# Performance work log

Hardware: AMD Instinct MI355X
Metric: run time of the kernel (lower is better)

## Reference

```python
import jax, jax.numpy as jnp
import numpy as np


def setup_inputs() -> dict:
    key = jax.random.key(0)
    kq, kk, kv = jax.random.split(key, 3)
    shape = (4, 16, 2048, 128)  # [B, H, S, D]
    return {
        "query": jax.random.normal(kq, shape, dtype=jnp.float32),
        "key": jax.random.normal(kk, shape, dtype=jnp.float32),
        "value": jax.random.normal(kv, shape, dtype=jnp.float32),
    }


def reference(query, key, value):
    # NOTE: the original torch code computes math.sqrt(d) but immediately
    # overwrites it with d itself, so the scale is 1/D (not 1/sqrt(D)).
    d = query.shape[-1]
    score = jnp.einsum("bhqd,bhkd->bhqk", query, key) / d  # [B,H,S,S]
    attn = jax.nn.softmax(score, axis=-1)
    return jnp.einsum("bhqk,bhkd->bhqd", attn, value)
```

## Files before the change

### kernel.cpp

```cpp
#include <hip/hip_runtime.h>
#include <stdint.h>

typedef __bf16 bf16x8 __attribute__((ext_vector_type(8)));
typedef __bf16 bf16x2 __attribute__((ext_vector_type(2)));
typedef float  f32x4  __attribute__((ext_vector_type(4)));

#define DEVI __device__ __forceinline__

constexpr int Bc = 4, Hc = 16, Ss = 2048, Dd = 128;
constexpr int BH = Bc * Hc;
constexpr int BM = 128;
constexpr int BN = 32;
constexpr int NTIL = Ss / BN;
constexpr int LDP = 40;
constexpr float SCALE = 1.0f / 128.0f;

constexpr int TILE_B = BN * Dd * 2;
constexpr int SK_OFF = 0;
constexpr int SV_OFF = 2 * TILE_B;
constexpr int SP_OFF = 4 * TILE_B;
constexpr int LDS_BYTES = SP_OFF + BM * LDP * 2;
static_assert(LDS_BYTES <= 54000, "need 3 blocks/CU");

DEVI unsigned short f2bf_bits(float x) {
  unsigned u = __builtin_bit_cast(unsigned, x);
  u += 0x7fffu + ((u >> 16) & 1u);
  return (unsigned short)(u >> 16);
}
DEVI __bf16 f2bf(float x) {
  unsigned short b = f2bf_bits(x);
  return __builtin_bit_cast(__bf16, b);
}

DEVI void gload_lds16(const void* g, void* l) {
  __builtin_amdgcn_global_load_lds(
      (const __attribute__((address_space(1))) unsigned*)(uintptr_t)g,
      (__attribute__((address_space(3))) unsigned*)(unsigned)(uintptr_t)l,
      16, 0, 0);
}

__global__ void k_conv_bf16(const float* __restrict__ in, __bf16* __restrict__ out,
                            int n4) {
  int i = blockIdx.x * blockDim.x + threadIdx.x;
  const int stride = gridDim.x * blockDim.x;
  for (; i < n4; i += stride) {
    float4 v = ((const float4*)in)[i];
    ushort4 o;
    o.x = f2bf_bits(v.x); o.y = f2bf_bits(v.y);
    o.z = f2bf_bits(v.z); o.w = f2bf_bits(v.w);
    ((ushort4*)out)[i] = o;
  }
}

__global__ void k_vtrans(const float* __restrict__ v, __bf16* __restrict__ vt) {
  constexpr int LDT = 130;
  __shared__ __bf16 tile[64 * LDT];
  const int bh = blockIdx.y;
  const int s0 = blockIdx.x * 64;
  const int u = threadIdx.x;
  const float4* src = (const float4*)(v + ((size_t)bh * Ss + s0) * Dd);
  #pragma unroll
  for (int i = 0; i < 8; i++) {
    int f = i * 256 + u;
    int row = f >> 5;
    int c4 = (f & 31) << 2;
    float4 x = src[f];
    tile[row * LDT + c4 + 0] = f2bf(x.x);
    tile[row * LDT + c4 + 1] = f2bf(x.y);
    tile[row * LDT + c4 + 2] = f2bf(x.z);
    tile[row * LDT + c4 + 3] = f2bf(x.w);
  }
  __syncthreads();
  const int c = u & 7;
  const int dl = u >> 3;
  #pragma unroll
  for (int it = 0; it < 4; it++) {
    const int d = it * 32 + dl;
    bf16x8 o;
    #pragma unroll
    for (int e = 0; e < 8; e++) o[e] = tile[(c * 8 + e) * LDT + d];
    *(bf16x8*)(vt + ((size_t)bh * Dd + d) * Ss + s0 + c * 8) = o;
  }
}

__launch_bounds__(256, 3)
__global__ void k_flash(const float* __restrict__ Q, const __bf16* __restrict__ Kb,
                        const __bf16* __restrict__ Vt, float* __restrict__ O) {
  __shared__ __align__(16) char lds[LDS_BYTES];
  unsigned short* sP = (unsigned short*)(lds + SP_OFF);

  const int tid = threadIdx.x;
  const int w = tid >> 6;
  const int lane = tid & 63;
  const int quad = lane >> 4;
  const int l16 = lane & 15;

  const int bx = blockIdx.x;
  const int bh = bx & (BH - 1);
  const int q0 = (bx >> 6) * BM;

  bf16x8 qa[2][4];
  {
    const float* qb = Q + ((size_t)bh * Ss + q0 + w * 32) * Dd;
    #pragma unroll
    for (int mt = 0; mt < 2; mt++)
      #pragma unroll
      for (int kk = 0; kk < 4; kk++) {
        const float* p = qb + (mt * 16 + l16) * Dd + kk * 32 + quad * 8;
        float4 a = ((const float4*)p)[0];
        float4 b = ((const float4*)p)[1];
        bf16x8 f;
        f[0] = f2bf(a.x * SCALE); f[1] = f2bf(a.y * SCALE);
        f[2] = f2bf(a.z * SCALE); f[3] = f2bf(a.w * SCALE);
        f[4] = f2bf(b.x * SCALE); f[5] = f2bf(b.y * SCALE);
        f[6] = f2bf(b.z * SCALE); f[7] = f2bf(b.w * SCALE);
        qa[mt][kk] = f;
      }
  }

  f32x4 acc[2][8];
  #pragma unroll
  for (int mt = 0; mt < 2; mt++)
    #pragma unroll
    for (int dt = 0; dt < 8; dt++)
      acc[mt][dt] = (f32x4){0.f, 0.f, 0.f, 0.f};

  float lacc[2] = {0.f, 0.f};

  const __bf16* kbh = Kb + (size_t)bh * Ss * Dd;
  const __bf16* vbh = Vt + (size_t)bh * Ss * Dd;

  const char* gp[4];
  unsigned lo[4];
  int ginc;
  if (w < 2) {
    #pragma unroll
    for (int i = 0; i < 4; i++) {
      const int fk = w * 4 + i, kk = fk >> 1, nt = fk & 1;
      gp[i] = (const char*)(kbh + (size_t)(nt * 16 + l16) * Dd + kk * 32 + quad * 8);
      lo[i] = (unsigned)(SK_OFF + fk * 1024 + lane * 16);
    }
    ginc = BN * Dd * 2;
  } else {
    #pragma unroll
    for (int i = 0; i < 4; i++) {
      const int dt = (w - 2) * 4 + i;
      gp[i] = (const char*)(vbh + (size_t)(dt * 16 + l16) * Ss + quad * 8);
      lo[i] = (unsigned)(SV_OFF + dt * 1024 + lane * 16);
    }
    ginc = BN * 2;
  }

  #pragma unroll
  for (int i = 0; i < 4; i++) gload_lds16(gp[i], lds + lo[i]);
  #pragma unroll
  for (int i = 0; i < 4; i++) gp[i] += ginc;
  __syncthreads();

  unsigned cur = 0;
  for (int t = 0; t < NTIL; t++) {
    if (t < NTIL - 1) {
      const unsigned nb = (cur ^ 1u) * (unsigned)TILE_B;
      #pragma unroll
      for (int i = 0; i < 4; i++) gload_lds16(gp[i], lds + lo[i] + nb);
      #pragma unroll
      for (int i = 0; i < 4; i++) gp[i] += ginc;
    }
    const char* bK = lds + SK_OFF + cur * TILE_B;
    const char* bV = lds + SV_OFF + cur * TILE_B;

    f32x4 sc[2][2];
    #pragma unroll
    for (int mt = 0; mt < 2; mt++)
      #pragma unroll
      for (int nt = 0; nt < 2; nt++)
        sc[mt][nt] = (f32x4){0.f, 0.f, 0.f, 0.f};
    __builtin_amdgcn_s_setprio(1);
    #pragma unroll
    for (int kk = 0; kk < 4; kk++)
      #pragma unroll
      for (int nt = 0; nt < 2; nt++) {
        bf16x8 bk = *(const bf16x8*)(bK + (kk * 2 + nt) * 1024 + lane * 16);
        sc[0][nt] = __builtin_amdgcn_mfma_f32_16x16x32_bf16(bk, qa[0][kk], sc[0][nt], 0, 0, 0);
        sc[1][nt] = __builtin_amdgcn_mfma_f32_16x16x32_bf16(bk, qa[1][kk], sc[1][nt], 0, 0, 0);
      }
    __builtin_amdgcn_s_setprio(0);

    #pragma unroll
    for (int mt = 0; mt < 2; mt++)
      #pragma unroll
      for (int nt = 0; nt < 2; nt++) {
        float p0 = __expf(sc[mt][nt][0]);
        float p1 = __expf(sc[mt][nt][1]);
        float p2 = __expf(sc[mt][nt][2]);
        float p3 = __expf(sc[mt][nt][3]);
        lacc[mt] += (p0 + p1) + (p2 + p3);
        bf16x2 ba, bb;
        ba[0] = (__bf16)p0; ba[1] = (__bf16)p1;
        bb[0] = (__bf16)p2; bb[1] = (__bf16)p3;
        uint2 pw;
        pw.x = __builtin_bit_cast(unsigned, ba);
        pw.y = __builtin_bit_cast(unsigned, bb);
        *(uint2*)(sP + (w * 32 + mt * 16 + l16) * LDP + nt * 16 + quad * 4) = pw;
      }

    bf16x8 pa[2];
    #pragma unroll
    for (int mt = 0; mt < 2; mt++)
      pa[mt] = *(const bf16x8*)((const char*)sP +
               (size_t)((w * 32 + mt * 16 + l16) * LDP + quad * 8) * 2);
    __builtin_amdgcn_s_setprio(1);
    #pragma unroll
    for (int dt = 0; dt < 8; dt++) {
      bf16x8 bv = *(const bf16x8*)(bV + dt * 1024 + lane * 16);
      acc[0][dt] = __builtin_amdgcn_mfma_f32_16x16x32_bf16(pa[0], bv, acc[0][dt], 0, 0, 0);
      acc[1][dt] = __builtin_amdgcn_mfma_f32_16x16x32_bf16(pa[1], bv, acc[1][dt], 0, 0, 0);
    }
    __builtin_amdgcn_s_setprio(0);

    __syncthreads();
    cur ^= 1u;
  }

  float inv_l[2][4];
  #pragma unroll
  for (int mt = 0; mt < 2; mt++) {
    float l = lacc[mt];
    l += __shfl_xor(l, 16);
    l += __shfl_xor(l, 32);
    #pragma unroll
    for (int r = 0; r < 4; r++) {
      float lr = __shfl(l, (lane & 48) | (quad * 4 + r));
      inv_l[mt][r] = 1.0f / lr;
    }
  }

  float* ob = O + ((size_t)bh * Ss + q0 + w * 32) * Dd;
  #pragma unroll
  for (int mt = 0; mt < 2; mt++)
    #pragma unroll
    for (int r = 0; r < 4; r++) {
      const float inv = inv_l[mt][r];
      const int row = mt * 16 + quad * 4 + r;
      #pragma unroll
      for (int dt = 0; dt < 8; dt++)
        ob[row * Dd + dt * 16 + l16] = acc[mt][dt][r] * inv;
    }
}

extern "C" void kernel_launch(void* const* d_in, const int* in_sizes, int n_in,
                              void* d_out, int out_size, void* d_ws, size_t ws_size,
                              hipStream_t stream) {
  const float* Q = (const float*)d_in[0];
  const float* K = (const float*)d_in[1];
  const float* V = (const float*)d_in[2];
  float* O = (float*)d_out;
  const size_t elems = (size_t)BH * Ss * Dd;
  __bf16* Kb = (__bf16*)d_ws;
  __bf16* Vt = Kb + elems;

  k_conv_bf16<<<4096, 256, 0, stream>>>(K, Kb, (int)(elems / 4));
  k_vtrans<<<dim3(Ss / 64, BH), 256, 0, stream>>>(V, Vt);
  k_flash<<<dim3((Ss / BM) * BH), 256, 0, stream>>>(Q, Kb, Vt, O);
}
```

Measured before the change: 363.2 us.

## Fuse prep kernels, swizzle P tile, use exp2 and target four blocks per CU

```diff
diff --git a/kernel.cpp b/kernel.cpp
--- a/kernel.cpp
+++ b/kernel.cpp
@@ -12,15 +12,14 @@
 constexpr int BM = 128;
 constexpr int BN = 32;
 constexpr int NTIL = Ss / BN;
-constexpr int LDP = 40;
-constexpr float SCALE = 1.0f / 128.0f;
+constexpr float SCALE = 1.44269504088896340736f / 128.0f;
 
 constexpr int TILE_B = BN * Dd * 2;
 constexpr int SK_OFF = 0;
 constexpr int SV_OFF = 2 * TILE_B;
 constexpr int SP_OFF = 4 * TILE_B;
-constexpr int LDS_BYTES = SP_OFF + BM * LDP * 2;
-static_assert(LDS_BYTES <= 54000, "need 3 blocks/CU");
+constexpr int LDS_BYTES = SP_OFF + BM * BN * 2;
+static_assert(LDS_BYTES <= 40960, "need 4 blocks/CU (160 KiB / 4)");
 
 DEVI unsigned short f2bf_bits(float x) {
   unsigned u = __builtin_bit_cast(unsigned, x);
@@ -31,6 +30,8 @@
   unsigned short b = f2bf_bits(x);
   return __builtin_bit_cast(__bf16, b);
 }
+
+DEVI float exp2_hw(float x) { return __builtin_amdgcn_exp2f(x); }
 
 DEVI void gload_lds16(const void* g, void* l) {
   __builtin_amdgcn_global_load_lds(
@@ -39,25 +40,28 @@
       16, 0, 0);
 }
 
-__global__ void k_conv_bf16(const float* __restrict__ in, __bf16* __restrict__ out,
-                            int n4) {
-  int i = blockIdx.x * blockDim.x + threadIdx.x;
-  const int stride = gridDim.x * blockDim.x;
-  for (; i < n4; i += stride) {
-    float4 v = ((const float4*)in)[i];
-    ushort4 o;
-    o.x = f2bf_bits(v.x); o.y = f2bf_bits(v.y);
-    o.z = f2bf_bits(v.z); o.w = f2bf_bits(v.w);
-    ((ushort4*)out)[i] = o;
-  }
-}
-
-__global__ void k_vtrans(const float* __restrict__ v, __bf16* __restrict__ vt) {
+__global__ void k_prep(const float* __restrict__ kin, __bf16* __restrict__ kout,
+                       const float* __restrict__ v, __bf16* __restrict__ vt) {
   constexpr int LDT = 130;
   __shared__ __bf16 tile[64 * LDT];
-  const int bh = blockIdx.y;
-  const int s0 = blockIdx.x * 64;
+  const int bx = blockIdx.x;
   const int u = threadIdx.x;
+  if (bx >= 2048) {
+    constexpr int N4 = (BH * Ss * Dd) / 4;
+    int i = (bx - 2048) * 256 + u;
+    const int stride = 2048 * 256;
+    #pragma unroll
+    for (int it = 0; it < N4 / (2048 * 256); it++, i += stride) {
+      float4 x = ((const float4*)kin)[i];
+      ushort4 o;
+      o.x = f2bf_bits(x.x); o.y = f2bf_bits(x.y);
+      o.z = f2bf_bits(x.z); o.w = f2bf_bits(x.w);
+      ((ushort4*)kout)[i] = o;
+    }
+    return;
+  }
+  const int bh = bx >> 5;
+  const int s0 = (bx & 31) * 64;
   const float4* src = (const float4*)(v + ((size_t)bh * Ss + s0) * Dd);
   #pragma unroll
   for (int i = 0; i < 8; i++) {
@@ -83,11 +87,11 @@
   }
 }
 
-__launch_bounds__(256, 3)
+__launch_bounds__(256, 4)
 __global__ void k_flash(const float* __restrict__ Q, const __bf16* __restrict__ Kb,
                         const __bf16* __restrict__ Vt, float* __restrict__ O) {
   __shared__ __align__(16) char lds[LDS_BYTES];
-  unsigned short* sP = (unsigned short*)(lds + SP_OFF);
+  char* sPB = lds + SP_OFF;
 
   const int tid = threadIdx.x;
   const int w = tid >> 6;
@@ -157,6 +161,8 @@
   for (int i = 0; i < 4; i++) gp[i] += ginc;
   __syncthreads();
 
+  const unsigned swz = (unsigned)(l16 & 3) << 4;
+
   unsigned cur = 0;
   for (int t = 0; t < NTIL; t++) {
     if (t < NTIL - 1) {
@@ -187,13 +193,14 @@
     __builtin_amdgcn_s_setprio(0);
 
     #pragma unroll
-    for (int mt = 0; mt < 2; mt++)
+    for (int mt = 0; mt < 2; mt++) {
+      const unsigned prow = (unsigned)((w * 32 + mt * 16 + l16) * 64);
       #pragma unroll
       for (int nt = 0; nt < 2; nt++) {
-        float p0 = __expf(sc[mt][nt][0]);
-        float p1 = __expf(sc[mt][nt][1]);
-        float p2 = __expf(sc[mt][nt][2]);
-        float p3 = __expf(sc[mt][nt][3]);
+        float p0 = exp2_hw(sc[mt][nt][0]);
+        float p1 = exp2_hw(sc[mt][nt][1]);
+        float p2 = exp2_hw(sc[mt][nt][2]);
+        float p3 = exp2_hw(sc[mt][nt][3]);
         lacc[mt] += (p0 + p1) + (p2 + p3);
         bf16x2 ba, bb;
         ba[0] = (__bf16)p0; ba[1] = (__bf16)p1;
@@ -201,14 +208,16 @@
         uint2 pw;
         pw.x = __builtin_bit_cast(unsigned, ba);
         pw.y = __builtin_bit_cast(unsigned, bb);
-        *(uint2*)(sP + (w * 32 + mt * 16 + l16) * LDP + nt * 16 + quad * 4) = pw;
+        *(uint2*)(sPB + prow + (((unsigned)(nt * 32 + quad * 8)) ^ swz)) = pw;
       }
+    }
 
     bf16x8 pa[2];
     #pragma unroll
-    for (int mt = 0; mt < 2; mt++)
-      pa[mt] = *(const bf16x8*)((const char*)sP +
-               (size_t)((w * 32 + mt * 16 + l16) * LDP + quad * 8) * 2);
+    for (int mt = 0; mt < 2; mt++) {
+      const unsigned prow = (unsigned)((w * 32 + mt * 16 + l16) * 64);
+      pa[mt] = *(const bf16x8*)(sPB + prow + (((unsigned)(quad * 16)) ^ swz));
+    }
     __builtin_amdgcn_s_setprio(1);
     #pragma unroll
     for (int dt = 0; dt < 8; dt++) {
@@ -259,7 +268,6 @@
   __bf16* Kb = (__bf16*)d_ws;
   __bf16* Vt = Kb + elems;
 
-  k_conv_bf16<<<4096, 256, 0, stream>>>(K, Kb, (int)(elems / 4));
-  k_vtrans<<<dim3(Ss / 64, BH), 256, 0, stream>>>(V, Vt);
+  k_prep<<<4096, 256, 0, stream>>>(K, Kb, V, Vt);
   k_flash<<<dim3((Ss / BM) * BH), 256, 0, stream>>>(Q, Kb, Vt, O);
 }
```

After: 524.0 us. 1.44x slower.
